# Kernel optimization log

Hardware: AMD Instinct MI355X
Metric: run time of the kernel (lower is better)

Reference implementation:

```python
import jax, jax.numpy as jnp
import numpy as np

DIM_M = 512
NEG_INF = -1e30


def setup_inputs() -> dict:
    key = jax.random.key(0)
    k1, k2, k3, k4, k5, k6, k7 = jax.random.split(key, 7)
    B, Lc, Lq, d = 16, 1024, 512, DIM_M
    C = jax.random.normal(k1, (B, Lc, d), dtype=jnp.float32)
    Q = jax.random.normal(k2, (B, Lq, d), dtype=jnp.float32)
    cmask = jax.random.randint(k3, (B, Lc), 0, 2).astype(jnp.float32)
    qmask = jax.random.randint(k4, (B, Lq), 0, 2).astype(jnp.float32)
    lim = np.sqrt(1.0 / d)
    w = jax.random.uniform(k5, (3 * d,), minval=-lim, maxval=lim, dtype=jnp.float32)
    # out_linear: Linear(4d -> d), torch default init
    bound = np.sqrt(1.0 / (4 * d))
    out_w = jax.random.uniform(k6, (d, 4 * d), minval=-bound, maxval=bound, dtype=jnp.float32)
    out_b = jax.random.uniform(k7, (d,), minval=-bound, maxval=bound, dtype=jnp.float32)
    return {"C": C, "Q": Q, "cmask": cmask, "qmask": qmask, "w": w, "out_w": out_w, "out_b": out_b}


def _mask_logits(t, m):
    return t * m + (1.0 - m) * NEG_INF


def reference(C, Q, cmask, qmask, w, out_w, out_b):
    d = C.shape[-1]
    w1, w2, w3 = w[:d], w[d:2 * d], w[2 * d:]
    # Decomposed trilinear similarity (same math as cat([Ct,Qt,Ct*Qt]) @ w):
    # S[b,i,j] = C[b,i]@w1 + Q[b,j]@w2 + (C[b,i]*w3) @ Q[b,j]
    S = (C @ w1)[:, :, None] + (Q @ w2)[:, None, :] \
        + jnp.einsum('bid,bjd->bij', C * w3, Q)  # [B, Lc, Lq]
    qm = qmask[:, None, :]  # [B, 1, Lq]
    cm = cmask[:, :, None]  # [B, Lc, 1]
    S1 = jax.nn.softmax(_mask_logits(S, qm), axis=2)  # over Lq
    S2 = jax.nn.softmax(_mask_logits(S, cm), axis=1)  # over Lc
    A = jnp.einsum('bij,bjd->bid', S1, Q)  # [B, Lc, d]
    # bmm(bmm(S1, S2^T), C) == S1 @ (S2^T @ C) by associativity (cheaper)
    S2TC = jnp.einsum('bij,bid->bjd', S2, C)  # [B, Lq, d]
    Bm = jnp.einsum('bij,bjd->bid', S1, S2TC)  # [B, Lc, d]
    out = jnp.concatenate([C, A, C * A, C * Bm], axis=2)  # [B, Lc, 4d]
    # dropout inactive (inference); out_linear
    return out @ out_w.T + out_b
```

## Files before the change

kernel.cpp:

```cpp
#include <hip/hip_runtime.h>
#include <hip/hip_bf16.h>


#define NB 16
#define LC 1024
#define LQ 512
#define DM 512
#define D4 2048
#define NEGINF (-1e30f)

typedef __bf16 v8bf __attribute__((ext_vector_type(8)));
typedef __bf16 v4bf __attribute__((ext_vector_type(4)));
typedef float  v4f  __attribute__((ext_vector_type(4)));

#define MFMA16 __builtin_amdgcn_mfma_f32_16x16x32_bf16

#define GLOAD16(gp, lp) __builtin_amdgcn_global_load_lds( \
    (const __attribute__((address_space(1))) void*)(gp), \
    (__attribute__((address_space(3))) void*)(lp), 16, 0, 0)

__device__ __forceinline__ void xcd_remap(int& bx, int& by, int& bz) {
  const int gx = gridDim.x, gy = gridDim.y, gz = gridDim.z;
  int flat = bx + gx * (by + gy * bz);
  int per = (gx * gy * gz) >> 3;
  int nw = (flat & 7) * per + (flat >> 3);
  bx = nw % gx;
  int r = nw / gx;
  by = r % gy;
  bz = r / gy;
}

#define P_PROLOG \
  __shared__ __bf16 Al[3][128 * 32], Bl[3][64 * 32]; \
  int bx = blockIdx.x, by = blockIdx.y, bz = blockIdx.z; \
  xcd_remap(bx, by, bz); \
  const int b = bz, i0 = by * 128, n0 = bx * 64; \
  const int t = threadIdx.x, lane = t & 63, wave = t >> 6; \
  const int wm = wave >> 1, wn = wave & 1, quad = lane >> 4, col = lane & 15; \
  const int srA = wave * 32 + (lane >> 2); \
  const int srB = wave * 16 + (lane >> 2); \
  const int swz = (((lane & 3) ^ ((lane >> 2) & 3) ^ ((lane >> 4) & 3)) * 8); \
  const int rdx = ((quad ^ (col & 3) ^ ((col >> 2) & 3)) * 8); \
  v4f acc[4][2]; \
  _Pragma("unroll") for (int x = 0; x < 4; ++x) \
  _Pragma("unroll") for (int y = 0; y < 2; ++y) \
  _Pragma("unroll") for (int r = 0; r < 4; ++r) acc[x][y][r] = 0.f;

#define P_STAGE(buf, Aptr, Bptr, LDGA, LDGB, k0) \
  do { \
    GLOAD16((Aptr) + (k0),                       &Al[buf][(wave * 32) * 32]); \
    GLOAD16((Aptr) + (size_t)16 * (LDGA) + (k0), &Al[buf][(wave * 32 + 16) * 32]); \
    GLOAD16((Bptr) + (k0),                       &Bl[buf][(wave * 16) * 32]); \
  } while (0)

#define P_COMPUTE(buf) \
  do { \
    v8bf af_[4], bf_[2]; \
    _Pragma("unroll") for (int x = 0; x < 4; ++x) \
      af_[x] = *(const v8bf*)&Al[buf][(wm * 64 + x * 16 + col) * 32 + rdx]; \
    _Pragma("unroll") for (int y = 0; y < 2; ++y) \
      bf_[y] = *(const v8bf*)&Bl[buf][(wn * 32 + y * 16 + col) * 32 + rdx]; \
    _Pragma("unroll") for (int x = 0; x < 4; ++x) \
    _Pragma("unroll") for (int y = 0; y < 2; ++y) \
      acc[x][y] = MFMA16(af_[x], bf_[y], acc[x][y], 0, 0, 0); \
  } while (0)

#define P_SYNC3() \
  do { asm volatile("s_waitcnt vmcnt(3)" ::: "memory"); \
       __builtin_amdgcn_s_barrier(); } while (0)
#define P_SYNC0() \
  do { asm volatile("s_waitcnt vmcnt(0)" ::: "memory"); \
       __builtin_amdgcn_s_barrier(); } while (0)

#define P_ROT() do { cur_ = (cur_ == 2) ? 0 : cur_ + 1; \
                     nx2_ = (nx2_ == 2) ? 0 : nx2_ + 1; } while (0)

#define P_KLOOP(Arow, Brow, LDGA, LDGB, KEXT) \
  { P_STAGE(0, Arow, Brow, LDGA, LDGB, 0); \
    P_STAGE(1, Arow, Brow, LDGA, LDGB, 32); \
    P_SYNC3(); \
    int cur_ = 0, nx2_ = 2; \
    for (int k0 = 0; k0 < (KEXT); k0 += 32) { \
      const int kn_ = k0 + 64; \
      if (kn_ < (KEXT)) { \
        P_STAGE(nx2_, Arow, Brow, LDGA, LDGB, kn_); \
        P_COMPUTE(cur_); \
        P_SYNC3(); \
      } else if (k0 + 32 < (KEXT)) { \
        P_COMPUTE(cur_); \
        P_SYNC0(); \
      } else { \
        P_COMPUTE(cur_); \
      } \
      P_ROT(); \
    } }

#define O_PROLOG \
  __shared__ __bf16 Al[3][128 * 32], Bl[3][128 * 32]; \
  int bx = blockIdx.x, by = blockIdx.y, bz = blockIdx.z; \
  xcd_remap(bx, by, bz); \
  const int b = bz, i0 = by * 128, n0 = bx * 128; \
  const int t = threadIdx.x, lane = t & 63, wave = t >> 6; \
  const int wm = wave >> 1, wn = wave & 1, quad = lane >> 4, col = lane & 15; \
  const int sr32 = wave * 32 + (lane >> 2); \
  const int swz = (((lane & 3) ^ ((lane >> 2) & 3) ^ ((lane >> 4) & 3)) * 8); \
  const int rdx = ((quad ^ (col & 3) ^ ((col >> 2) & 3)) * 8); \
  v4f acc[4][4]; \
  _Pragma("unroll") for (int x = 0; x < 4; ++x) \
  _Pragma("unroll") for (int y = 0; y < 4; ++y) \
  _Pragma("unroll") for (int r = 0; r < 4; ++r) acc[x][y][r] = 0.f;

#define O_STAGE(buf, Aptr, Bptr, LDGA, LDGB, k0) \
  do { \
    GLOAD16((Aptr) + (k0),                       &Al[buf][(wave * 32) * 32]); \
    GLOAD16((Aptr) + (size_t)16 * (LDGA) + (k0), &Al[buf][(wave * 32 + 16) * 32]); \
    GLOAD16((Bptr) + (k0),                       &Bl[buf][(wave * 32) * 32]); \
    GLOAD16((Bptr) + (size_t)16 * (LDGB) + (k0), &Bl[buf][(wave * 32 + 16) * 32]); \
  } while (0)

#define O_COMPUTE(buf) \
  do { \
    v8bf af_[4], bf_[4]; \
    _Pragma("unroll") for (int x = 0; x < 4; ++x) \
      af_[x] = *(const v8bf*)&Al[buf][(wm * 64 + x * 16 + col) * 32 + rdx]; \
    _Pragma("unroll") for (int y = 0; y < 4; ++y) \
      bf_[y] = *(const v8bf*)&Bl[buf][(wn * 64 + y * 16 + col) * 32 + rdx]; \
    _Pragma("unroll") for (int x = 0; x < 4; ++x) \
    _Pragma("unroll") for (int y = 0; y < 4; ++y) \
      acc[x][y] = MFMA16(af_[x], bf_[y], acc[x][y], 0, 0, 0); \
  } while (0)

#define O_SYNC4() \
  do { asm volatile("s_waitcnt vmcnt(4)" ::: "memory"); \
       __builtin_amdgcn_s_barrier(); } while (0)
#define O_SYNC0() \
  do { asm volatile("s_waitcnt vmcnt(0)" ::: "memory"); \
       __builtin_amdgcn_s_barrier(); } while (0)

#define O_ROT() do { cur_ = (cur_ == 2) ? 0 : cur_ + 1; \
                     nx2_ = (nx2_ == 2) ? 0 : nx2_ + 1; } while (0)

__global__ void k_rowdots(const float* __restrict__ C, const float* __restrict__ Q,
                          const float* __restrict__ w,
                          float* __restrict__ cw1, float* __restrict__ qw2,
                          __bf16* __restrict__ Cbf, __bf16* __restrict__ Qw3) {
  const int wid = threadIdx.x >> 6, lane = threadIdx.x & 63;
  const int row = blockIdx.x * 4 + wid;
  const bool isC = row < NB * LC;
  const int lr = isC ? row : row - NB * LC;
  const float* src = (isC ? C : Q) + (size_t)lr * DM;
  const float* wv  = isC ? w : (w + DM);
  const float* w3  = w + 2 * DM;
  __bf16* dst = (isC ? Cbf : Qw3) + (size_t)lr * DM;
  float v = 0.f;
#pragma unroll
  for (int s = 0; s < 2; ++s) {
    const int k = lane * 4 + s * 256;
    float4 f = *(const float4*)(src + k);
    float4 g = *(const float4*)(wv + k);
    v += f.x * g.x + f.y * g.y + f.z * g.z + f.w * g.w;
    v4bf h;
    if (isC) {
      h[0] = (__bf16)f.x; h[1] = (__bf16)f.y; h[2] = (__bf16)f.z; h[3] = (__bf16)f.w;
    } else {
      float4 s3 = *(const float4*)(w3 + k);
      h[0] = (__bf16)(f.x * s3.x); h[1] = (__bf16)(f.y * s3.y);
      h[2] = (__bf16)(f.z * s3.z); h[3] = (__bf16)(f.w * s3.w);
    }
    *(v4bf*)(dst + k) = h;
  }
#pragma unroll
  for (int off = 32; off; off >>= 1) v += __shfl_down(v, off, 64);
  if (lane == 0) {
    if (isC) cw1[row] = v;
    else     qw2[lr] = v;
  }
}

__device__ __forceinline__ void transpose_tile_f32(const float* __restrict__ in,
                                                   __bf16* __restrict__ outT,
                                                   int R, int Cd, int tbx, int tby, int tb) {
  __shared__ __bf16 tile[64][66];
  const int r0 = tby * 64, c0 = tbx * 64;
  const int tr = threadIdx.x >> 6, tc = threadIdx.x & 63;
  const float* inb = in + (size_t)tb * R * Cd;
  __bf16* outb = outT + (size_t)tb * Cd * R;
  for (int r = tr; r < 64; r += 4)
    tile[r][tc] = (__bf16)inb[(size_t)(r0 + r) * Cd + c0 + tc];
  __syncthreads();
  for (int c = tr; c < 64; c += 4)
    outb[(size_t)(c0 + c) * R + r0 + tc] = tile[tc][c];
}

__device__ __forceinline__ void transpose_tile_bf(const __bf16* __restrict__ in,
                                                  __bf16* __restrict__ outT,
                                                  int R, int Cd, int tbx, int tby, int tb) {
  __shared__ __bf16 tile[64][66];
  const int r0 = tby * 64, c0 = tbx * 64;
  const int tr = threadIdx.x >> 6, tc = threadIdx.x & 63;
  const __bf16* inb = in + (size_t)tb * R * Cd;
  __bf16* outb = outT + (size_t)tb * Cd * R;
  for (int r = tr; r < 64; r += 4)
    tile[r][tc] = inb[(size_t)(r0 + r) * Cd + c0 + tc];
  __syncthreads();
  for (int c = tr; c < 64; c += 4)
    outb[(size_t)(c0 + c) * R + r0 + tc] = tile[tc][c];
}

__global__ void k_prep(const float* __restrict__ C, const __bf16* __restrict__ Cbf,
                       const float* __restrict__ Q, const float* __restrict__ OW,
                       __bf16* __restrict__ CT, __bf16* __restrict__ QT,
                       __bf16* __restrict__ OWb, int use_cbf) {
  const int id = blockIdx.x;
  if (id < 2048) {
    if (use_cbf) transpose_tile_bf(Cbf, CT, LC, DM, id & 7, (id >> 3) & 15, id >> 7);
    else         transpose_tile_f32(C,  CT, LC, DM, id & 7, (id >> 3) & 15, id >> 7);
  } else if (id < 3072) {
    const int id2 = id - 2048;
    transpose_tile_f32(Q, QT, LQ, DM, id2 & 7, (id2 >> 3) & 7, id2 >> 6);
  } else {
    const size_t i = ((size_t)(id - 3072) * 256 + threadIdx.x) * 4;
    float4 f = *(const float4*)(OW + i);
    v4bf h; h[0] = (__bf16)f.x; h[1] = (__bf16)f.y; h[2] = (__bf16)f.z; h[3] = (__bf16)f.w;
    *(v4bf*)(OWb + i) = h;
  }
}

__global__ void k_cvt2b(const float* __restrict__ Cf, const float* __restrict__ OW,
                        __bf16* __restrict__ Cb3, __bf16* __restrict__ OWb) {
  const size_t NC = (size_t)NB * LC * DM;
  size_t i = ((size_t)blockIdx.x * 256 + threadIdx.x) * 4;
  if (i < NC) {
    float4 f = *(const float4*)(Cf + i);
    v4bf h; h[0] = (__bf16)f.x; h[1] = (__bf16)f.y; h[2] = (__bf16)f.z; h[3] = (__bf16)f.w;
    *(v4bf*)(Cb3 + i) = h;
  } else {
    size_t j = i - NC;
    float4 f = *(const float4*)(OW + j);
    v4bf h; h[0] = (__bf16)f.x; h[1] = (__bf16)f.y; h[2] = (__bf16)f.z; h[3] = (__bf16)f.w;
    *(v4bf*)(OWb + j) = h;
  }
}

__global__ __launch_bounds__(256) void k_mfma_S(
    const __bf16* __restrict__ Cbf, const __bf16* __restrict__ Qw3,
    const float* __restrict__ cw1, const float* __restrict__ qw2,
    float* __restrict__ S) {
  P_PROLOG
  const __bf16* Arow = Cbf + (size_t)b * LC * DM + (size_t)(i0 + srA) * DM + swz;
  const __bf16* Brow = Qw3 + (size_t)b * LQ * DM + (size_t)(n0 + srB) * DM + swz;
  P_KLOOP(Arow, Brow, DM, DM, DM)
  float* Sb = S + (size_t)b * LC * LQ;
#pragma unroll
  for (int x = 0; x < 4; ++x) {
    const int mB = i0 + wm * 64 + x * 16 + quad * 4;
    float cv[4];
#pragma unroll
    for (int r = 0; r < 4; ++r) cv[r] = cw1[b * LC + mB + r];
#pragma unroll
    for (int y = 0; y < 2; ++y) {
      const int j = n0 + wn * 32 + y * 16 + col;
      const float qv = qw2[b * LQ + j];
#pragma unroll
      for (int r = 0; r < 4; ++r)
        Sb[(size_t)(mB + r) * LQ + j] = acc[x][y][r] + cv[r] + qv;
    }
  }
}

__global__ __launch_bounds__(1024) void k_softstat(
    const float* __restrict__ S, const float* __restrict__ qmask,
    const float* __restrict__ cmask, __bf16* __restrict__ S1,
    float2* __restrict__ pstat) {
  __shared__ float2 cst[16][LQ];
  const int b = blockIdx.y, ic = blockIdx.x;
  const int tid = threadIdx.x, wv = tid >> 6, lane = tid & 63;
  const float* qm  = qmask + b * LQ;
  const float* cm  = cmask + b * LC + ic * 64;
  const float* Sb  = S  + ((size_t)b * LC + ic * 64) * LQ;
  __bf16*      S1b = S1 + ((size_t)b * LC + ic * 64) * LQ;
  float colm[8], cols[8];
#pragma unroll
  for (int tt = 0; tt < 8; ++tt) { colm[tt] = -3e38f; cols[tt] = 0.f; }
  for (int it = 0; it < 4; ++it) {
    const int r = wv * 4 + it;
    const float cmv = cm[r];
    const float* Srow = Sb + (size_t)r * LQ;
    float sv[8], l1[8];
    float m = -3e38f;
#pragma unroll
    for (int tt = 0; tt < 8; ++tt) {
      int j = lane + 64 * tt;
      sv[tt] = Srow[j];
      float qv = qm[j];
      l1[tt] = qv * sv[tt] + (1.f - qv) * NEGINF;
      m = fmaxf(m, l1[tt]);
    }
#pragma unroll
    for (int off = 32; off; off >>= 1) m = fmaxf(m, __shfl_xor(m, off, 64));
    float e[8], s = 0.f;
#pragma unroll
    for (int tt = 0; tt < 8; ++tt) { e[tt] = __expf(l1[tt] - m); s += e[tt]; }
#pragma unroll
    for (int off = 32; off; off >>= 1) s += __shfl_xor(s, off, 64);
    const float inv = 1.f / s;
#pragma unroll
    for (int tt = 0; tt < 8; ++tt)
      S1b[(size_t)r * LQ + lane + 64 * tt] = (__bf16)(e[tt] * inv);
    if (cmv != 0.f) {
#pragma unroll
      for (int tt = 0; tt < 8; ++tt) {
        float l2 = sv[tt];
        if (l2 > colm[tt]) { cols[tt] *= __expf(colm[tt] - l2); colm[tt] = l2; }
        cols[tt] += __expf(l2 - colm[tt]);
      }
    }
  }
#pragma unroll
  for (int tt = 0; tt < 8; ++tt) cst[wv][lane + 64 * tt] = make_float2(colm[tt], cols[tt]);
  __syncthreads();
  if (tid < LQ) {
    float M = -3e38f, Sd = 0.f;
#pragma unroll
    for (int k = 0; k < 16; ++k) {
      float2 p = cst[k][tid];
      float nM = fmaxf(M, p.x);
      Sd = Sd * __expf(M - nM) + p.y * __expf(p.x - nM);
      M = nM;
    }
    pstat[((size_t)(b * 16 + ic) * LQ) + tid] = make_float2(M, Sd);
  }
}

__global__ void k_colwrite(const float* __restrict__ S, const float* __restrict__ cmask,
                           const float2* __restrict__ pstat, __bf16* __restrict__ S2T) {
  __shared__ float Mf[64], If[64];
  __shared__ __bf16 tile[64][66];
  const int b = blockIdx.z, ic = blockIdx.y, j0 = blockIdx.x * 64;
  const int c = threadIdx.x & 63, ip = threadIdx.x >> 6;
  if (threadIdx.x < 64) {
    float M = -3e38f, Sd = 0.f;
#pragma unroll
    for (int k = 0; k < 16; ++k) {
      float2 p = pstat[((size_t)(b * 16 + k) * LQ) + j0 + threadIdx.x];
      float nM = fmaxf(M, p.x);
      Sd = Sd * __expf(M - nM) + p.y * __expf(p.x - nM);
      M = nM;
    }
    Mf[threadIdx.x] = M; If[threadIdx.x] = 1.f / Sd;
  }
  __syncthreads();
  const float M = Mf[c], inv = If[c];
  const float* Sb = S + ((size_t)b * LC + ic * 64) * LQ;
  const float* cm = cmask + b * LC + ic * 64;
  for (int r = ip; r < 64; r += 4) {
    if (cm[r] != 0.f)
      tile[r][c] = (__bf16)(__expf(Sb[(size_t)r * LQ + j0 + c] - M) * inv);
    else
      tile[r][c] = (__bf16)0.f;
  }
  __syncthreads();
  __bf16* S2Tb = S2T + ((size_t)b * LQ + j0) * LC + ic * 64;
  for (int jr = ip; jr < 64; jr += 4)
    S2Tb[(size_t)jr * LC + c] = tile[c][jr];
}

__global__ __launch_bounds__(256) void k_mfma_A(
    const __bf16* __restrict__ S1, const __bf16* __restrict__ QT,
    const float* __restrict__ Cf, __bf16* __restrict__ Aw, __bf16* __restrict__ CAw) {
  P_PROLOG
  const __bf16* Arow = S1 + (size_t)b * LC * LQ + (size_t)(i0 + srA) * LQ + swz;
  const __bf16* Brow = QT + (size_t)b * DM * LQ + (size_t)(n0 + srB) * LQ + swz;
  P_KLOOP(Arow, Brow, LQ, LQ, LQ)
  const float* Cb = Cf + (size_t)b * LC * DM;
  __bf16* Ab  = Aw  + (size_t)b * LC * DM;
  __bf16* CAb = CAw + (size_t)b * LC * DM;
#pragma unroll
  for (int x = 0; x < 4; ++x) {
    const int mB = i0 + wm * 64 + x * 16 + quad * 4;
#pragma unroll
    for (int y = 0; y < 2; ++y) {
      const int n = n0 + wn * 32 + y * 16 + col;
#pragma unroll
      for (int r = 0; r < 4; ++r) {
        const float av = acc[x][y][r];
        const float cv = Cb[(size_t)(mB + r) * DM + n];
        Ab[(size_t)(mB + r) * DM + n]  = (__bf16)av;
        CAb[(size_t)(mB + r) * DM + n] = (__bf16)(av * cv);
      }
    }
  }
}

__global__ __launch_bounds__(256) void k_mfma_T(
    const __bf16* __restrict__ S2T, const __bf16* __restrict__ CT, __bf16* __restrict__ S2TCT) {
  P_PROLOG
  const int j0 = i0;
  const __bf16* Arow = S2T + (size_t)b * LQ * LC + (size_t)(j0 + srA) * LC + swz;
  const __bf16* Brow = CT  + (size_t)b * DM * LC + (size_t)(n0 + srB) * LC + swz;
  P_KLOOP(Arow, Brow, LC, LC, LC)
#pragma unroll
  for (int x = 0; x < 4; ++x) {
    const int jB = j0 + wm * 64 + x * 16 + quad * 4;
#pragma unroll
    for (int y = 0; y < 2; ++y) {
      const int n = n0 + wn * 32 + y * 16 + col;
      v4bf h;
#pragma unroll
      for (int r = 0; r < 4; ++r) h[r] = (__bf16)acc[x][y][r];
      *(v4bf*)&S2TCT[((size_t)b * DM + n) * LQ + jB] = h;
    }
  }
}

__global__ __launch_bounds__(256) void k_mfma_Bm(
    const __bf16* __restrict__ S1, const __bf16* __restrict__ S2TCT,
    const float* __restrict__ Cf, __bf16* __restrict__ CBw) {
  P_PROLOG
  const __bf16* Arow = S1    + (size_t)b * LC * LQ + (size_t)(i0 + srA) * LQ + swz;
  const __bf16* Brow = S2TCT + (size_t)b * DM * LQ + (size_t)(n0 + srB) * LQ + swz;
  P_KLOOP(Arow, Brow, LQ, LQ, LQ)
  const float* Cb = Cf + (size_t)b * LC * DM;
  __bf16* CBb = CBw + (size_t)b * LC * DM;
#pragma unroll
  for (int x = 0; x < 4; ++x) {
    const int mB = i0 + wm * 64 + x * 16 + quad * 4;
#pragma unroll
    for (int y = 0; y < 2; ++y) {
      const int n = n0 + wn * 32 + y * 16 + col;
#pragma unroll
      for (int r = 0; r < 4; ++r) {
        const float cv = Cb[(size_t)(mB + r) * DM + n];
        CBb[(size_t)(mB + r) * DM + n] = (__bf16)(acc[x][y][r] * cv);
      }
    }
  }
}

__global__ __launch_bounds__(256) void k_mfma_out(
    const __bf16* __restrict__ Cb3, const __bf16* __restrict__ Aw,
    const __bf16* __restrict__ CAw, const __bf16* __restrict__ CBw,
    const __bf16* __restrict__ OWb, const float* __restrict__ ob,
    float* __restrict__ out) {
  O_PROLOG
  const size_t rowoff = (size_t)b * LC * DM + (size_t)(i0 + sr32) * DM + swz;
  const __bf16* Aseg[4] = {Cb3 + rowoff, Aw + rowoff, CAw + rowoff, CBw + rowoff};
  const __bf16* Brow0 = OWb + (size_t)(n0 + sr32) * D4 + swz;
  O_STAGE(0, Aseg[0], Brow0, DM, D4, 0);
  O_STAGE(1, Aseg[0], Brow0, DM, D4, 32);
  O_SYNC4();
  int cur_ = 0, nx2_ = 2;
#pragma unroll
  for (int seg = 0; seg < 4; ++seg) {
    const __bf16* Ac = Aseg[seg];
    const __bf16* An = Aseg[seg < 3 ? seg + 1 : 3];
    const __bf16* Bc = Brow0 + seg * DM;
    const __bf16* Bn = Brow0 + (seg < 3 ? seg + 1 : 3) * DM;
    for (int j = 0; j < 14; ++j) {
      O_STAGE(nx2_, Ac, Bc, DM, D4, (j + 2) * 32);
      O_COMPUTE(cur_);
      O_SYNC4();
      O_ROT();
    }
    if (seg < 3) {
      O_STAGE(nx2_, An, Bn, DM, D4, 0);
      O_COMPUTE(cur_);
      O_SYNC4();
      O_ROT();
      O_STAGE(nx2_, An, Bn, DM, D4, 32);
      O_COMPUTE(cur_);
      O_SYNC4();
      O_ROT();
    } else {
      O_COMPUTE(cur_);
      O_SYNC0();
      O_ROT();
      O_COMPUTE(cur_);
    }
  }
  float* outb = out + (size_t)b * LC * DM;
#pragma unroll
  for (int x = 0; x < 4; ++x) {
    const int mB = i0 + wm * 64 + x * 16 + quad * 4;
#pragma unroll
    for (int y = 0; y < 4; ++y) {
      const int n = n0 + wn * 64 + y * 16 + col;
      const float bv = ob[n];
#pragma unroll
      for (int r = 0; r < 4; ++r)
        outb[(size_t)(mB + r) * DM + n] = acc[x][y][r] + bv;
    }
  }
}

extern "C" void kernel_launch(void* const* d_in, const int* in_sizes, int n_in,
                              void* d_out, int out_size, void* d_ws, size_t ws_size,
                              hipStream_t stream) {
  const float* C     = (const float*)d_in[0];
  const float* Q     = (const float*)d_in[1];
  const float* cmask = (const float*)d_in[2];
  const float* qmask = (const float*)d_in[3];
  const float* w     = (const float*)d_in[4];
  const float* out_w = (const float*)d_in[5];
  const float* out_b = (const float*)d_in[6];
  float* out = (float*)d_out;

  char* base = (char*)d_ws;
  float*  cw1   = (float*)base;
  float*  qw2   = (float*)(base + 65536);
  char*   R     = base + 131072;
  float*  S     = (float*)R;
  __bf16* CT    = (__bf16*)R;
  __bf16* Aw    = (__bf16*)R;
  __bf16* QT    = (__bf16*)(R + (16u << 20));
  __bf16* CBw   = (__bf16*)(R + (16u << 20));
  __bf16* S1    = (__bf16*)(R + (32u << 20));
  __bf16* Qw3   = (__bf16*)(R + (48u << 20));
  __bf16* S2T   = (__bf16*)(R + (48u << 20));
  __bf16* CAw   = (__bf16*)(R + (48u << 20));
  float2* pstat = (float2*)(R + (64u << 20));
  __bf16* S2TCT = (__bf16*)(R + (64u << 20));
  (void)in_sizes; (void)n_in; (void)out_size;

  const size_t need_big = 131072 + (90ull << 20);
  const bool bigws = ws_size >= need_big;

  __bf16 *Cbf, *Cbf3, *OWbf;
  if (bigws) {
    Cbf  = (__bf16*)(R + (72u << 20));
    Cbf3 = Cbf;
    OWbf = (__bf16*)(R + (88u << 20));
  } else {
    Cbf  = (__bf16*)(R + (32u << 20));
    Cbf3 = (__bf16*)(R + (32u << 20));
    OWbf = (__bf16*)(R + (64u << 20));
  }

  k_rowdots<<<(NB * LC + NB * LQ) / 4, 256, 0, stream>>>(C, Q, w, cw1, qw2, Cbf, Qw3);
  k_mfma_S<<<dim3(LQ / 64, LC / 128, NB), 256, 0, stream>>>(Cbf, Qw3, cw1, qw2, S);
  k_softstat<<<dim3(LC / 64, NB), 1024, 0, stream>>>(S, qmask, cmask, S1, pstat);
  k_colwrite<<<dim3(LQ / 64, LC / 64, NB), 256, 0, stream>>>(S, cmask, pstat, S2T);
  k_prep<<<bigws ? 4096 : 3072, 256, 0, stream>>>(C, Cbf, Q, out_w, CT, QT, OWbf,
                                                  bigws ? 1 : 0);
  k_mfma_T<<<dim3(DM / 64, LQ / 128, NB), 256, 0, stream>>>(S2T, CT, S2TCT);
  k_mfma_A<<<dim3(DM / 64, LC / 128, NB), 256, 0, stream>>>(S1, QT, C, Aw, CAw);
  k_mfma_Bm<<<dim3(DM / 64, LC / 128, NB), 256, 0, stream>>>(S1, S2TCT, C, CBw);
  if (!bigws)
    k_cvt2b<<<(NB * LC * DM + DM * D4) / 1024, 256, 0, stream>>>(C, out_w, Cbf3, OWbf);
  k_mfma_out<<<dim3(DM / 128, LC / 128, NB), 256, 0, stream>>>(Cbf3, Aw, CAw, CBw, OWbf, out_b, out);
}
```

Baseline: 269.4 us.

## Restructure P-kernel K-loop into paired stages, add MFMA priority, read bf16 C in epilogues

The P-family GEMM K-loop moves from a 3-buffer rotating pipeline to a 4-buffer scheme. Each iteration loads two 32-wide K stages together and computes two stages per barrier, which halves the barrier count. It now waits with vmcnt(0) each pair, so prefetch depth may effectively shrink. The out GEMM raises wave priority around its MFMA block. The A and Bm epilogues read C from the bf16 copy when the big workspace is present, halving epilogue C traffic at slight precision cost.

```diff
diff --git a/kernel.cpp b/kernel.cpp
--- a/kernel.cpp
+++ b/kernel.cpp
@@ -31,7 +31,7 @@
 }
 
 #define P_PROLOG \
-  __shared__ __bf16 Al[3][128 * 32], Bl[3][64 * 32]; \
+  __shared__ __bf16 Al[4][128 * 32], Bl[4][64 * 32]; \
   int bx = blockIdx.x, by = blockIdx.y, bz = blockIdx.z; \
   xcd_remap(bx, by, bz); \
   const int b = bz, i0 = by * 128, n0 = bx * 64; \
@@ -46,11 +46,11 @@
   _Pragma("unroll") for (int y = 0; y < 2; ++y) \
   _Pragma("unroll") for (int r = 0; r < 4; ++r) acc[x][y][r] = 0.f;
 
-#define P_STAGE(buf, Aptr, Bptr, LDGA, LDGB, k0) \
+#define P_STAGE1(s, Aptr, Bptr, LDGA, LDGB, k0) \
   do { \
-    GLOAD16((Aptr) + (k0),                       &Al[buf][(wave * 32) * 32]); \
-    GLOAD16((Aptr) + (size_t)16 * (LDGA) + (k0), &Al[buf][(wave * 32 + 16) * 32]); \
-    GLOAD16((Bptr) + (k0),                       &Bl[buf][(wave * 16) * 32]); \
+    GLOAD16((Aptr) + (k0),                       &Al[s][(wave * 32) * 32]); \
+    GLOAD16((Aptr) + (size_t)16 * (LDGA) + (k0), &Al[s][(wave * 32 + 16) * 32]); \
+    GLOAD16((Bptr) + (k0),                       &Bl[s][(wave * 16) * 32]); \
   } while (0)
 
 #define P_COMPUTE(buf) \
@@ -65,34 +65,21 @@
       acc[x][y] = MFMA16(af_[x], bf_[y], acc[x][y], 0, 0, 0); \
   } while (0)
 
-#define P_SYNC3() \
-  do { asm volatile("s_waitcnt vmcnt(3)" ::: "memory"); \
-       __builtin_amdgcn_s_barrier(); } while (0)
-#define P_SYNC0() \
-  do { asm volatile("s_waitcnt vmcnt(0)" ::: "memory"); \
-       __builtin_amdgcn_s_barrier(); } while (0)
-
-#define P_ROT() do { cur_ = (cur_ == 2) ? 0 : cur_ + 1; \
-                     nx2_ = (nx2_ == 2) ? 0 : nx2_ + 1; } while (0)
-
 #define P_KLOOP(Arow, Brow, LDGA, LDGB, KEXT) \
-  { P_STAGE(0, Arow, Brow, LDGA, LDGB, 0); \
-    P_STAGE(1, Arow, Brow, LDGA, LDGB, 32); \
-    P_SYNC3(); \
-    int cur_ = 0, nx2_ = 2; \
-    for (int k0 = 0; k0 < (KEXT); k0 += 32) { \
-      const int kn_ = k0 + 64; \
-      if (kn_ < (KEXT)) { \
-        P_STAGE(nx2_, Arow, Brow, LDGA, LDGB, kn_); \
-        P_COMPUTE(cur_); \
-        P_SYNC3(); \
-      } else if (k0 + 32 < (KEXT)) { \
-        P_COMPUTE(cur_); \
-        P_SYNC0(); \
-      } else { \
-        P_COMPUTE(cur_); \
+  { P_STAGE1(0, Arow, Brow, LDGA, LDGB, 0); \
+    P_STAGE1(1, Arow, Brow, LDGA, LDGB, 32); \
+    const int np_ = (KEXT) / 64; \
+    for (int q = 0; q < np_; ++q) { \
+      asm volatile("s_waitcnt vmcnt(0)" ::: "memory"); \
+      __builtin_amdgcn_s_barrier(); \
+      const int s0_ = (2 * q) & 3, s1_ = s0_ + 1; \
+      if (q + 1 < np_) { \
+        const int t0_ = (2 * q + 2) & 3, t1_ = t0_ + 1; \
+        P_STAGE1(t0_, Arow, Brow, LDGA, LDGB, (q + 1) * 64); \
+        P_STAGE1(t1_, Arow, Brow, LDGA, LDGB, (q + 1) * 64 + 32); \
       } \
-      P_ROT(); \
+      P_COMPUTE(s0_); \
+      P_COMPUTE(s1_); \
     } }
 
 #define O_PROLOG \
@@ -125,9 +112,11 @@
       af_[x] = *(const v8bf*)&Al[buf][(wm * 64 + x * 16 + col) * 32 + rdx]; \
     _Pragma("unroll") for (int y = 0; y < 4; ++y) \
       bf_[y] = *(const v8bf*)&Bl[buf][(wn * 64 + y * 16 + col) * 32 + rdx]; \
+    __builtin_amdgcn_s_setprio(1); \
     _Pragma("unroll") for (int x = 0; x < 4; ++x) \
     _Pragma("unroll") for (int y = 0; y < 4; ++y) \
       acc[x][y] = MFMA16(af_[x], bf_[y], acc[x][y], 0, 0, 0); \
+    __builtin_amdgcn_s_setprio(0); \
   } while (0)
 
 #define O_SYNC4() \
@@ -367,26 +356,46 @@
 
 __global__ __launch_bounds__(256) void k_mfma_A(
     const __bf16* __restrict__ S1, const __bf16* __restrict__ QT,
-    const float* __restrict__ Cf, __bf16* __restrict__ Aw, __bf16* __restrict__ CAw) {
+    const float* __restrict__ Cf, const __bf16* __restrict__ Cbfp, int use_cbf,
+    __bf16* __restrict__ Aw, __bf16* __restrict__ CAw) {
   P_PROLOG
   const __bf16* Arow = S1 + (size_t)b * LC * LQ + (size_t)(i0 + srA) * LQ + swz;
   const __bf16* Brow = QT + (size_t)b * DM * LQ + (size_t)(n0 + srB) * LQ + swz;
   P_KLOOP(Arow, Brow, LQ, LQ, LQ)
-  const float* Cb = Cf + (size_t)b * LC * DM;
   __bf16* Ab  = Aw  + (size_t)b * LC * DM;
   __bf16* CAb = CAw + (size_t)b * LC * DM;
-#pragma unroll
-  for (int x = 0; x < 4; ++x) {
-    const int mB = i0 + wm * 64 + x * 16 + quad * 4;
-#pragma unroll
-    for (int y = 0; y < 2; ++y) {
-      const int n = n0 + wn * 32 + y * 16 + col;
-#pragma unroll
-      for (int r = 0; r < 4; ++r) {
-        const float av = acc[x][y][r];
-        const float cv = Cb[(size_t)(mB + r) * DM + n];
-        Ab[(size_t)(mB + r) * DM + n]  = (__bf16)av;
-        CAb[(size_t)(mB + r) * DM + n] = (__bf16)(av * cv);
+  if (use_cbf) {
+    const __bf16* Cb = Cbfp + (size_t)b * LC * DM;
+#pragma unroll
+    for (int x = 0; x < 4; ++x) {
+      const int mB = i0 + wm * 64 + x * 16 + quad * 4;
+#pragma unroll
+      for (int y = 0; y < 2; ++y) {
+        const int n = n0 + wn * 32 + y * 16 + col;
+#pragma unroll
+        for (int r = 0; r < 4; ++r) {
+          const float av = acc[x][y][r];
+          const float cv = (float)Cb[(size_t)(mB + r) * DM + n];
+          Ab[(size_t)(mB + r) * DM + n]  = (__bf16)av;
+          CAb[(size_t)(mB + r) * DM + n] = (__bf16)(av * cv);
+        }
+      }
+    }
+  } else {
+    const float* Cb = Cf + (size_t)b * LC * DM;
+#pragma unroll
+    for (int x = 0; x < 4; ++x) {
+      const int mB = i0 + wm * 64 + x * 16 + quad * 4;
+#pragma unroll
+      for (int y = 0; y < 2; ++y) {
+        const int n = n0 + wn * 32 + y * 16 + col;
+#pragma unroll
+        for (int r = 0; r < 4; ++r) {
+          const float av = acc[x][y][r];
+          const float cv = Cb[(size_t)(mB + r) * DM + n];
+          Ab[(size_t)(mB + r) * DM + n]  = (__bf16)av;
+          CAb[(size_t)(mB + r) * DM + n] = (__bf16)(av * cv);
+        }
       }
     }
   }
@@ -415,23 +424,41 @@
 
 __global__ __launch_bounds__(256) void k_mfma_Bm(
     const __bf16* __restrict__ S1, const __bf16* __restrict__ S2TCT,
-    const float* __restrict__ Cf, __bf16* __restrict__ CBw) {
+    const float* __restrict__ Cf, const __bf16* __restrict__ Cbfp, int use_cbf,
+    __bf16* __restrict__ CBw) {
   P_PROLOG
   const __bf16* Arow = S1    + (size_t)b * LC * LQ + (size_t)(i0 + srA) * LQ + swz;
   const __bf16* Brow = S2TCT + (size_t)b * DM * LQ + (size_t)(n0 + srB) * LQ + swz;
   P_KLOOP(Arow, Brow, LQ, LQ, LQ)
-  const float* Cb = Cf + (size_t)b * LC * DM;
   __bf16* CBb = CBw + (size_t)b * LC * DM;
-#pragma unroll
-  for (int x = 0; x < 4; ++x) {
-    const int mB = i0 + wm * 64 + x * 16 + quad * 4;
-#pragma unroll
-    for (int y = 0; y < 2; ++y) {
-      const int n = n0 + wn * 32 + y * 16 + col;
-#pragma unroll
-      for (int r = 0; r < 4; ++r) {
-        const float cv = Cb[(size_t)(mB + r) * DM + n];
-        CBb[(size_t)(mB + r) * DM + n] = (__bf16)(acc[x][y][r] * cv);
+  if (use_cbf) {
+    const __bf16* Cb = Cbfp + (size_t)b * LC * DM;
+#pragma unroll
+    for (int x = 0; x < 4; ++x) {
+      const int mB = i0 + wm * 64 + x * 16 + quad * 4;
+#pragma unroll
+      for (int y = 0; y < 2; ++y) {
+        const int n = n0 + wn * 32 + y * 16 + col;
+#pragma unroll
+        for (int r = 0; r < 4; ++r) {
+          const float cv = (float)Cb[(size_t)(mB + r) * DM + n];
+          CBb[(size_t)(mB + r) * DM + n] = (__bf16)(acc[x][y][r] * cv);
+        }
+      }
+    }
+  } else {
+    const float* Cb = Cf + (size_t)b * LC * DM;
+#pragma unroll
+    for (int x = 0; x < 4; ++x) {
+      const int mB = i0 + wm * 64 + x * 16 + quad * 4;
+#pragma unroll
+      for (int y = 0; y < 2; ++y) {
+        const int n = n0 + wn * 32 + y * 16 + col;
+#pragma unroll
+        for (int r = 0; r < 4; ++r) {
+          const float cv = Cb[(size_t)(mB + r) * DM + n];
+          CBb[(size_t)(mB + r) * DM + n] = (__bf16)(acc[x][y][r] * cv);
+        }
       }
     }
   }
@@ -535,16 +562,16 @@
     Cbf3 = (__bf16*)(R + (32u << 20));
     OWbf = (__bf16*)(R + (64u << 20));
   }
+  const int ucb = bigws ? 1 : 0;
 
   k_rowdots<<<(NB * LC + NB * LQ) / 4, 256, 0, stream>>>(C, Q, w, cw1, qw2, Cbf, Qw3);
   k_mfma_S<<<dim3(LQ / 64, LC / 128, NB), 256, 0, stream>>>(Cbf, Qw3, cw1, qw2, S);
   k_softstat<<<dim3(LC / 64, NB), 1024, 0, stream>>>(S, qmask, cmask, S1, pstat);
   k_colwrite<<<dim3(LQ / 64, LC / 64, NB), 256, 0, stream>>>(S, cmask, pstat, S2T);
-  k_prep<<<bigws ? 4096 : 3072, 256, 0, stream>>>(C, Cbf, Q, out_w, CT, QT, OWbf,
-                                                  bigws ? 1 : 0);
+  k_prep<<<bigws ? 4096 : 3072, 256, 0, stream>>>(C, Cbf, Q, out_w, CT, QT, OWbf, ucb);
   k_mfma_T<<<dim3(DM / 64, LQ / 128, NB), 256, 0, stream>>>(S2T, CT, S2TCT);
-  k_mfma_A<<<dim3(DM / 64, LC / 128, NB), 256, 0, stream>>>(S1, QT, C, Aw, CAw);
-  k_mfma_Bm<<<dim3(DM / 64, LC / 128, NB), 256, 0, stream>>>(S1, S2TCT, C, CBw);
+  k_mfma_A<<<dim3(DM / 64, LC / 128, NB), 256, 0, stream>>>(S1, QT, C, Cbf3, ucb, Aw, CAw);
+  k_mfma_Bm<<<dim3(DM / 64, LC / 128, NB), 256, 0, stream>>>(S1, S2TCT, C, Cbf3, ucb, CBw);
   if (!bigws)
     k_cvt2b<<<(NB * LC * DM + DM * D4) / 1024, 256, 0, stream>>>(C, out_w, Cbf3, OWbf);
   k_mfma_out<<<dim3(DM / 128, LC / 128, NB), 256, 0, stream>>>(Cbf3, Aw, CAw, CBw, OWbf, out_b, out);
```

After: 277.6 us. 3.0% more time.
